# Optimization experiments

Hardware: AMD Instinct MI355X
Metric: run time of the kernel (lower is better)

## Reference

```python
import jax, jax.numpy as jnp
import numpy as np

NUM_HEADS = 8

def mha(q, k, v, in_w, in_b, out_w, out_b):
    # q:[B,Lq,E] k,v:[B,Lk,E]; torch nn.MultiheadAttention math (batch_first)
    B, Lq, E = q.shape
    Lk = k.shape[1]
    H = NUM_HEADS
    D = E // H
    wq, wk, wv = in_w[:E], in_w[E:2*E], in_w[2*E:]      # each [E,E], torch layout [out,in]
    bq, bk, bv = in_b[:E], in_b[E:2*E], in_b[2*E:]
    qp = (q @ wq.T + bq).reshape(B, Lq, H, D)
    kp = (k @ wk.T + bk).reshape(B, Lk, H, D)
    vp = (v @ wv.T + bv).reshape(B, Lk, H, D)
    scores = jnp.einsum('bqhd,bkhd->bhqk', qp, kp) / jnp.sqrt(jnp.asarray(D, q.dtype))
    attn = jax.nn.softmax(scores, axis=-1)
    ctx = jnp.einsum('bhqk,bkhd->bqhd', attn, vp).reshape(B, Lq, E)
    return ctx @ out_w.T + out_b

def setup_inputs() -> dict:
    key = jax.random.key(0)
    ks = jax.random.split(key, 12)
    B, IN, E, M, NB = 2048, 1024, 512, 256, 8
    s = lambda *d: 1.0 / np.sqrt(d[-1])
    return {
        'x':      jax.random.normal(ks[0], (B, IN), jnp.float32),
        'memory': jax.random.uniform(ks[1], (M, E), jnp.float32, -s(E), s(E)),
        'enc_w':  jax.random.uniform(ks[2], (E, IN), jnp.float32, -s(IN), s(IN)),
        'enc_b':  jnp.zeros((E,), jnp.float32),
        'blk_w':  jax.random.uniform(ks[3], (NB, E, E), jnp.float32, -s(E), s(E)),
        'blk_b':  jnp.zeros((NB, E), jnp.float32),
        'in_w':   jax.random.uniform(ks[4], (3 * E, E), jnp.float32, -s(E), s(E)),
        'in_b':   jnp.zeros((3 * E,), jnp.float32),
        'out_w':  jax.random.uniform(ks[5], (E, E), jnp.float32, -s(E), s(E)),
        'out_b':  jnp.zeros((E,), jnp.float32),
        'dec_w':  jax.random.uniform(ks[6], (IN, E), jnp.float32, -s(E), s(E)),
        'dec_b':  jnp.zeros((IN,), jnp.float32),
    }

def reference(x, memory, enc_w, enc_b, blk_w, blk_b, in_w, in_b, out_w, out_b, dec_w, dec_b):
    B = x.shape[0]
    encoded = jnp.tanh(x @ enc_w.T + enc_b)                     # [B,E]
    # all block linears at once: [B, NB, E]
    memory_updates = jnp.einsum('be,noe->bno', encoded, blk_w) + blk_b
    mem = jnp.broadcast_to(memory[None], (B,) + memory.shape)   # [B,M,E]
    attended = mha(memory_updates, mem, mem, in_w, in_b, out_w, out_b)
    updated_memory = mem + jnp.mean(attended, axis=1, keepdims=True)
    retrieved = mha(encoded[:, None, :], updated_memory, updated_memory, in_w, in_b, out_w, out_b)
    output = retrieved[:, 0, :] @ dec_w.T + dec_b               # [B,IN]
    return output, updated_memory
```

## Files before the change

### kernel.cpp

```cpp
#include <hip/hip_runtime.h>
#include <math.h>


typedef __attribute__((ext_vector_type(8))) short short8;
typedef __attribute__((ext_vector_type(4))) float f32x4;
typedef unsigned short u16;

__device__ inline u16 bf16_rn(float x) {
    unsigned u = __float_as_uint(x);
    unsigned r = (u + 0x7FFFu + ((u >> 16) & 1u)) >> 16;
    return (u16)r;
}
__device__ inline float bf16_f(u16 h) { return __uint_as_float(((unsigned)h) << 16); }

__global__ __launch_bounds__(256)
void prep_all(const float* __restrict__ x, const float* __restrict__ mm,
              const float* __restrict__ ew, const float* __restrict__ iw,
              const float* __restrict__ ow, const float* __restrict__ dw,
              const float* __restrict__ blk_w,
              const float* __restrict__ in_b, const float* __restrict__ blk_b,
              const float* __restrict__ out_b, const float* __restrict__ dec_b,
              u16* __restrict__ xh, u16* __restrict__ xl,
              u16* __restrict__ mh, u16* __restrict__ ml,
              u16* __restrict__ ewh, u16* __restrict__ ewl,
              u16* __restrict__ iwh, u16* __restrict__ iwl,
              u16* __restrict__ owh, u16* __restrict__ owl,
              u16* __restrict__ dwh, u16* __restrict__ dwl,
              u16* __restrict__ bwTh, u16* __restrict__ bwTl,
              u16* __restrict__ owTh, u16* __restrict__ owTl,
              float* __restrict__ bias1, float* __restrict__ bias2,
              float* __restrict__ bias_uv)
{
    __shared__ float T[32][33];
    const int id = blockIdx.x;
    const int t = threadIdx.x;
    if (id < 2304) {
        const int z = id >> 8, within = id & 255;
        const float* s; u16 *dh, *dl;
        if (z < 8) { s = blk_w + (long long)z * 262144;
                     dh = bwTh + (long long)z * 262144; dl = bwTl + (long long)z * 262144; }
        else       { s = ow; dh = owTh; dl = owTl; }
        const int c0 = (within & 15) * 32, r0 = (within >> 4) * 32;
        const int tx = t & 31, ty = t >> 5;
        #pragma unroll
        for (int rr = 0; rr < 4; ++rr)
            T[ty + rr * 8][tx] = s[(long long)(r0 + ty + rr * 8) * 512 + c0 + tx];
        __syncthreads();
        #pragma unroll
        for (int rr = 0; rr < 4; ++rr) {
            float v = T[tx][ty + rr * 8];
            long long o = (long long)(c0 + ty + rr * 8) * 512 + r0 + tx;
            u16 hh = bf16_rn(v);
            dh[o] = hh; dl[o] = bf16_rn(v - bf16_f(hh));
        }
    } else if (id < 2326) {
        int idx = (id - 2304) * 256 + t;
        if (idx < 4096) {
            int n = idx >> 9, f = idx & 511;
            const float* wr_ = iw + (long long)f * 512;
            const float* bb  = blk_b + n * 512;
            float s = in_b[f];
            for (int o = 0; o < 512; ++o) s += wr_[o] * bb[o];
            bias1[idx] = s;
        } else if (idx < 5120) {
            int i = idx - 4096;
            const float* dr = dw + (long long)i * 512;
            float s = dec_b[i];
            for (int f = 0; f < 512; ++f) s += dr[f] * out_b[f];
            bias2[i] = s;
        } else if (idx < 5632) {
            int f = idx - 5120;
            const float* wv = iw + (long long)(1024 + f) * 512;
            float s = 0.f;
            for (int e = 0; e < 512; ++e) s += wv[e] * out_b[e];
            bias_uv[f] = s;
        }
    } else {
        const long long total = 1081344;
        const long long stride = 2048LL * 256;
        for (long long i = (long long)(id - 2326) * 256 + t; i < total; i += stride) {
            const float* src; u16 *hi, *lo; long long j;
            if (i < 524288)      { src = x;  hi = xh;  lo = xl;  j = i; }
            else if (i < 557056) { src = mm; hi = mh;  lo = ml;  j = i - 524288; }
            else if (i < 688128) { src = ew; hi = ewh; lo = ewl; j = i - 557056; }
            else if (i < 884736) { src = iw; hi = iwh; lo = iwl; j = i - 688128; }
            else if (i < 950272) { src = ow; hi = owh; lo = owl; j = i - 884736; }
            else                 { src = dw; hi = dwh; lo = dwl; j = i - 950272; }
            float4 v = reinterpret_cast<const float4*>(src)[j];
            u16 h0 = bf16_rn(v.x), h1 = bf16_rn(v.y), h2 = bf16_rn(v.z), h3 = bf16_rn(v.w);
            ushort4 hv = {h0, h1, h2, h3};
            ushort4 lv = {bf16_rn(v.x - bf16_f(h0)), bf16_rn(v.y - bf16_f(h1)),
                          bf16_rn(v.z - bf16_f(h2)), bf16_rn(v.w - bf16_f(h3))};
            reinterpret_cast<ushort4*>(hi)[j] = hv;
            reinterpret_cast<ushort4*>(lo)[j] = lv;
        }
    }
}

struct ZD {
    const u16 *Ah, *Al, *Bh, *Bl;
    const float* bias;
    float* Cf; u16 *Ch, *Cl;
    int M, lda, ldb, ldc, K, act, omode;
    float scale;
};
template<int NZ> struct ZPack { ZD d[NZ]; };

__device__ __forceinline__ void gemm_zd(const ZD& dz, int m0, int n0,
    u16 (*Ash)[40], u16 (*Asl)[40], u16 (*Bsh)[40], u16 (*Bsl)[40])
{
    const int t  = threadIdx.x;
    const int r  = t >> 2;
    const int ck = (t & 3) << 3;
    const int lane = t & 63;
    const int wid  = t >> 6;
    const int wr = (wid >> 1) * 64;
    const int wc = (wid & 1) * 32;
    const int lr = lane & 15;
    const int lk = (lane >> 4) << 3;

    f32x4 acc[4][2];
    const f32x4 zero = {0.f, 0.f, 0.f, 0.f};
    #pragma unroll
    for (int i = 0; i < 4; ++i)
        #pragma unroll
        for (int j = 0; j < 2; ++j) acc[i][j] = zero;

    const long long arow0 = (long long)(m0 + r) * dz.lda;
    const long long arow1 = (long long)(m0 + r + 64) * dz.lda;
    const long long brow  = (long long)(n0 + r) * dz.ldb;

    for (int k0 = 0; k0 < dz.K; k0 += 32) {
        int4 vah0 = *reinterpret_cast<const int4*>(dz.Ah + arow0 + k0 + ck);
        int4 vah1 = *reinterpret_cast<const int4*>(dz.Ah + arow1 + k0 + ck);
        int4 val0 = *reinterpret_cast<const int4*>(dz.Al + arow0 + k0 + ck);
        int4 val1 = *reinterpret_cast<const int4*>(dz.Al + arow1 + k0 + ck);
        int4 vbh  = *reinterpret_cast<const int4*>(dz.Bh + brow  + k0 + ck);
        int4 vbl  = *reinterpret_cast<const int4*>(dz.Bl + brow  + k0 + ck);
        __syncthreads();
        *reinterpret_cast<int4*>(&Ash[r][ck])      = vah0;
        *reinterpret_cast<int4*>(&Ash[r + 64][ck]) = vah1;
        *reinterpret_cast<int4*>(&Asl[r][ck])      = val0;
        *reinterpret_cast<int4*>(&Asl[r + 64][ck]) = val1;
        *reinterpret_cast<int4*>(&Bsh[r][ck])      = vbh;
        *reinterpret_cast<int4*>(&Bsl[r][ck])      = vbl;
        __syncthreads();

        short8 fah[4], fal[4], fbh[2], fbl[2];
        #pragma unroll
        for (int i = 0; i < 4; ++i) {
            fah[i] = *reinterpret_cast<const short8*>(&Ash[wr + i * 16 + lr][lk]);
            fal[i] = *reinterpret_cast<const short8*>(&Asl[wr + i * 16 + lr][lk]);
        }
        #pragma unroll
        for (int j = 0; j < 2; ++j) {
            fbh[j] = *reinterpret_cast<const short8*>(&Bsh[wc + j * 16 + lr][lk]);
            fbl[j] = *reinterpret_cast<const short8*>(&Bsl[wc + j * 16 + lr][lk]);
        }
        #pragma unroll
        for (int i = 0; i < 4; ++i)
            #pragma unroll
            for (int j = 0; j < 2; ++j) {
                acc[i][j] = __builtin_amdgcn_mfma_f32_16x16x32_bf16(fah[i], fbh[j], acc[i][j], 0, 0, 0);
                acc[i][j] = __builtin_amdgcn_mfma_f32_16x16x32_bf16(fah[i], fbl[j], acc[i][j], 0, 0, 0);
                acc[i][j] = __builtin_amdgcn_mfma_f32_16x16x32_bf16(fal[i], fbh[j], acc[i][j], 0, 0, 0);
            }
    }

    #pragma unroll
    for (int j = 0; j < 2; ++j) {
        const int col = n0 + wc + j * 16 + lr;
        const float bv = dz.bias ? dz.bias[col] : 0.f;
        #pragma unroll
        for (int i = 0; i < 4; ++i) {
            #pragma unroll
            for (int q = 0; q < 4; ++q) {
                const int row = m0 + wr + i * 16 + ((lane >> 4) << 2) + q;
                float v = (acc[i][j][q] + bv) * dz.scale;
                if (dz.act) v = tanhf(v);
                if (dz.omode == 0) {
                    dz.Cf[(long long)row * dz.ldc + col] = v;
                } else {
                    long long off = (dz.omode == 1)
                        ? (long long)row * dz.ldc + col
                        : (long long)col * dz.ldc + row;
                    u16 h = bf16_rn(v);
                    dz.Ch[off] = h;
                    dz.Cl[off] = bf16_rn(v - bf16_f(h));
                }
            }
        }
    }
}

template<int NZ>
__global__ __launch_bounds__(256)
void gemm_multi(ZPack<NZ> pk)
{
    __shared__ u16 Ash[128][40];
    __shared__ u16 Asl[128][40];
    __shared__ u16 Bsh[64][40];
    __shared__ u16 Bsl[64][40];
    const ZD dz = pk.d[blockIdx.z];
    const int m0 = blockIdx.x * 128;
    if (m0 >= dz.M) return;
    gemm_zd(dz, m0, blockIdx.y * 64, Ash, Asl, Bsh, Bsl);
}

template<int MODE>
__device__ __forceinline__ void attn_body(char* smem, int bxblk, int h,
    const u16* __restrict__ Qph, const u16* __restrict__ Qpl,
    const u16* __restrict__ Kvh, const u16* __restrict__ Kvl,
    const u16* __restrict__ VTh, const u16* __restrict__ VTl,
    const float* __restrict__ uv, u16* __restrict__ Oh, u16* __restrict__ Ol)
{
    const int t = threadIdx.x;
    const int lane = t & 63, w = t >> 6;
    const int l15 = lane & 15, g = lane >> 4;
    const int wr = w * 32;
    const int b0 = bxblk * (MODE == 0 ? 16 : 128);

    u16* Qs = (u16*)smem;
    char* KsB = smem + 36864;

    for (int c = t; c < 2048; c += 256) {
        int plane = c >> 10, rem = c & 1023;
        int row = rem >> 3, seg = rem & 7;
        const u16* src = plane ? Qpl : Qph;
        long long addr;
        if (MODE == 0) {
            int q = row >> 4, bb = row & 15;
            addr = ((long long)q * 2048 + b0 + bb) * 512 + h * 64 + seg * 8;
        } else {
            addr = (long long)(b0 + row) * 512 + h * 64 + seg * 8;
        }
        *(int4*)(&Qs[plane * 9216 + row * 72 + seg * 8]) = *(const int4*)(src + addr);
    }

    f32x4 sacc[2][16];
    const f32x4 zero = {0.f, 0.f, 0.f, 0.f};
    #pragma unroll
    for (int i = 0; i < 2; ++i)
        #pragma unroll
        for (int j = 0; j < 16; ++j) sacc[i][j] = zero;

    short8 qfh[2][2], qfl[2][2];

    for (int kh = 0; kh < 2; ++kh) {
        if (kh) __syncthreads();
        for (int c = t; c < 2048; c += 256) {
            int plane = c >> 10, rem = c & 1023;
            int key = rem >> 3, seg = rem & 7;
            const u16* src = plane ? Kvl : Kvh;
            *(int4*)(KsB + plane * 18432 + key * 144 + seg * 16) =
                *(const int4*)(src + (long long)(kh * 128 + key) * 1024 + h * 64 + seg * 8);
        }
        __syncthreads();
        if (kh == 0) {
            #pragma unroll
            for (int i = 0; i < 2; ++i)
                #pragma unroll
                for (int kf = 0; kf < 2; ++kf) {
                    int ro = (wr + 16 * i + l15) * 72 + kf * 32 + g * 8;
                    qfh[i][kf] = *(const short8*)(&Qs[ro]);
                    qfl[i][kf] = *(const short8*)(&Qs[9216 + ro]);
                }
        }
        #pragma unroll
        for (int j = 0; j < 8; ++j) {
            int jg = kh * 8 + j;
            #pragma unroll
            for (int kf = 0; kf < 2; ++kf) {
                const char* kb = KsB + (j * 16 + l15) * 144 + (kf * 32 + g * 8) * 2;
                short8 kbh = *(const short8*)(kb);
                short8 kbl = *(const short8*)(kb + 18432);
                #pragma unroll
                for (int i = 0; i < 2; ++i) {
                    sacc[i][jg] = __builtin_amdgcn_mfma_f32_16x16x32_bf16(qfh[i][kf], kbh, sacc[i][jg], 0, 0, 0);
                    sacc[i][jg] = __builtin_amdgcn_mfma_f32_16x16x32_bf16(qfh[i][kf], kbl, sacc[i][jg], 0, 0, 0);
                    sacc[i][jg] = __builtin_amdgcn_mfma_f32_16x16x32_bf16(qfl[i][kf], kbh, sacc[i][jg], 0, 0, 0);
                }
            }
        }
    }

    float inv[2][4];
    #pragma unroll
    for (int i = 0; i < 2; ++i)
        #pragma unroll
        for (int q = 0; q < 4; ++q) {
            float m = -1e30f;
            #pragma unroll
            for (int j = 0; j < 16; ++j) m = fmaxf(m, sacc[i][j][q]);
            #pragma unroll
            for (int off = 1; off <= 8; off <<= 1) m = fmaxf(m, __shfl_xor(m, off, 64));
            #pragma unroll
            for (int j = 0; j < 16; ++j) sacc[i][j][q] = __expf(sacc[i][j][q] - m);
            float s = 0.f;
            #pragma unroll
            for (int j = 0; j < 16; ++j) s += sacc[i][j][q];
            #pragma unroll
            for (int off = 1; off <= 8; off <<= 1) s += __shfl_xor(s, off, 64);
            inv[i][q] = 1.0f / s;
        }

    f32x4 ctx[2][4];
    #pragma unroll
    for (int i = 0; i < 2; ++i)
        #pragma unroll
        for (int jd = 0; jd < 4; ++jd) ctx[i][jd] = zero;

    for (int qt = 0; qt < 4; ++qt) {
        __syncthreads();
        #pragma unroll
        for (int i = 0; i < 2; ++i)
            #pragma unroll
            for (int jj = 0; jj < 4; ++jj) {
                int jg = qt * 4 + jj;
                #pragma unroll
                for (int q = 0; q < 4; ++q) {
                    int row = wr + 16 * i + 4 * g + q;
                    int key = jj * 16 + l15;
                    float pv = sacc[i][jg][q];
                    u16 ph = bf16_rn(pv);
                    u16 pl = bf16_rn(pv - bf16_f(ph));
                    int byt = row * 128 + ((key * 2) ^ ((row & 7) << 4));
                    *(u16*)(smem + byt) = ph;
                    *(u16*)(smem + 16384 + byt) = pl;
                }
            }
        for (int c = t; c < 1024; c += 256) {
            int plane = c >> 9, rem = c & 511;
            int d = rem >> 3, seg = rem & 7;
            const u16* src = plane ? VTl : VTh;
            int4 v = *(const int4*)(src + (long long)h * 16384 + d * 256 + qt * 64 + seg * 8);
            int byt = 36864 + plane * 8192 + d * 128 + ((seg * 16) ^ ((d & 7) << 4));
            *(int4*)(smem + byt) = v;
        }
        __syncthreads();

        short8 pah[2][2], pal[2][2];
        #pragma unroll
        for (int i = 0; i < 2; ++i)
            #pragma unroll
            for (int kf = 0; kf < 2; ++kf) {
                int row = wr + 16 * i + l15;
                int byt = row * 128 + ((kf * 64 + g * 16) ^ ((row & 7) << 4));
                pah[i][kf] = *(const short8*)(smem + byt);
                pal[i][kf] = *(const short8*)(smem + 16384 + byt);
            }
        #pragma unroll
        for (int jd = 0; jd < 4; ++jd) {
            #pragma unroll
            for (int kf = 0; kf < 2; ++kf) {
                int d = 16 * jd + l15;
                int byt = 36864 + d * 128 + ((kf * 64 + g * 16) ^ ((d & 7) << 4));
                short8 vbh = *(const short8*)(smem + byt);
                short8 vbl = *(const short8*)(smem + 8192 + byt);
                #pragma unroll
                for (int i = 0; i < 2; ++i) {
                    ctx[i][jd] = __builtin_amdgcn_mfma_f32_16x16x32_bf16(pah[i][kf], vbh, ctx[i][jd], 0, 0, 0);
                    ctx[i][jd] = __builtin_amdgcn_mfma_f32_16x16x32_bf16(pah[i][kf], vbl, ctx[i][jd], 0, 0, 0);
                    ctx[i][jd] = __builtin_amdgcn_mfma_f32_16x16x32_bf16(pal[i][kf], vbh, ctx[i][jd], 0, 0, 0);
                }
            }
        }
    }

    if (MODE == 0) {
        __syncthreads();
        float* R = (float*)smem;
        #pragma unroll
        for (int i = 0; i < 2; ++i)
            #pragma unroll
            for (int jd = 0; jd < 4; ++jd)
                #pragma unroll
                for (int q = 0; q < 4; ++q) {
                    int qa = 2 * w + i;
                    int bb = 4 * g + q;
                    int d  = 16 * jd + l15;
                    R[qa * 1024 + bb * 64 + d] = ctx[i][jd][q] * inv[i][q];
                }
        __syncthreads();
        for (int o = t; o < 1024; o += 256) {
            int bb = o >> 6, d = o & 63;
            float s = 0.f;
            #pragma unroll
            for (int qa = 0; qa < 8; ++qa) s += R[qa * 1024 + bb * 64 + d];
            s *= 0.125f;
            long long addr = (long long)(b0 + bb) * 512 + h * 64 + d;
            u16 hh = bf16_rn(s);
            Oh[addr] = hh;
            Ol[addr] = bf16_rn(s - bf16_f(hh));
        }
    } else {
        #pragma unroll
        for (int i = 0; i < 2; ++i)
            #pragma unroll
            for (int jd = 0; jd < 4; ++jd)
                #pragma unroll
                for (int q = 0; q < 4; ++q) {
                    int b = b0 + wr + 16 * i + 4 * g + q;
                    int d = 16 * jd + l15;
                    long long addr = (long long)b * 512 + h * 64 + d;
                    float v = ctx[i][jd][q] * inv[i][q] + uv[addr];
                    u16 hh = bf16_rn(v);
                    Oh[addr] = hh;
                    Ol[addr] = bf16_rn(v - bf16_f(hh));
                }
    }
}

template<int MODE>
__global__ __launch_bounds__(256, 2)
void fused_attn(const u16* __restrict__ Qph, const u16* __restrict__ Qpl,
                const u16* __restrict__ Kvh, const u16* __restrict__ Kvl,
                const u16* __restrict__ VTh, const u16* __restrict__ VTl,
                const float* __restrict__ uv,
                u16* __restrict__ Oh, u16* __restrict__ Ol)
{
    extern __shared__ char smem[];
    attn_body<MODE>(smem, blockIdx.x, blockIdx.y, Qph, Qpl, Kvh, Kvl,
                    VTh, VTl, uv, Oh, Ol);
}

__device__ __forceinline__ void write_half(int wb, int half,
    const float* __restrict__ mem, const float* __restrict__ u,
    float* __restrict__ out1)
{
    const float4* m4 = reinterpret_cast<const float4*>(mem);
    const float4* u4 = reinterpret_cast<const float4*>(u);
    float4* o4 = reinterpret_cast<float4*>(out1);
    long long i0 = (long long)half * 33554432 + (long long)wb * 16384 + threadIdx.x;
    #pragma unroll 4
    for (int j = 0; j < 64; ++j) {
        long long i = i0 + j * 256;
        int e4 = (int)(i & 127);
        int m  = (int)((i >> 7) & 255);
        long long b = i >> 15;
        float4 a = m4[m * 128 + e4];
        float4 c = u4[b * 128 + e4];
        float4 rr = {a.x + c.x, a.y + c.y, a.z + c.z, a.w + c.w};
        o4[i] = rr;
    }
}

__global__ __launch_bounds__(256, 2)
void attn1_write(const u16* __restrict__ Qph, const u16* __restrict__ Qpl,
                 const u16* __restrict__ Kvh, const u16* __restrict__ Kvl,
                 const u16* __restrict__ VTh, const u16* __restrict__ VTl,
                 const float* __restrict__ uv,
                 u16* __restrict__ Oh, u16* __restrict__ Ol,
                 const float* __restrict__ mem, const float* __restrict__ uf,
                 float* __restrict__ out1)
{
    extern __shared__ char smem[];
    const int id = blockIdx.x;
    if (id < 128) {
        attn_body<1>(smem, id >> 3, id & 7, Qph, Qpl, Kvh, Kvl, VTh, VTl,
                     uv, Oh, Ol);
    } else {
        write_half(id - 128, 0, mem, uf, out1);
    }
}

__global__ __launch_bounds__(256)
void final_write(const u16* __restrict__ c2h, const u16* __restrict__ c2l,
                 const u16* __restrict__ W2h, const u16* __restrict__ W2l,
                 const float* __restrict__ bias2, float* __restrict__ out,
                 const float* __restrict__ mem, const float* __restrict__ uf,
                 float* __restrict__ out1)
{
    __shared__ u16 Ash[128][40];
    __shared__ u16 Asl[128][40];
    __shared__ u16 Bsh[64][40];
    __shared__ u16 Bsl[64][40];
    const int id = blockIdx.x;
    if (id < 256) {
        ZD dz = { c2h, c2l, W2h, W2l, bias2, out, nullptr, nullptr,
                  2048, 512, 512, 1024, 512, 0, 0, 1.0f };
        gemm_zd(dz, (id & 15) * 128, (id >> 4) * 64, Ash, Asl, Bsh, Bsl);
    } else {
        write_half(id - 256, 1, mem, uf, out1);
    }
}

extern "C" void kernel_launch(void* const* d_in, const int* in_sizes, int n_in,
                              void* d_out, int out_size, void* d_ws, size_t ws_size,
                              hipStream_t stream)
{
    (void)in_sizes; (void)n_in; (void)out_size; (void)ws_size;
    const float* x     = (const float*)d_in[0];
    const float* mem   = (const float*)d_in[1];
    const float* enc_w = (const float*)d_in[2];
    const float* enc_b = (const float*)d_in[3];
    const float* blk_w = (const float*)d_in[4];
    const float* blk_b = (const float*)d_in[5];
    const float* in_w  = (const float*)d_in[6];
    const float* in_b  = (const float*)d_in[7];
    const float* out_w = (const float*)d_in[8];
    const float* out_b = (const float*)d_in[9];
    const float* dec_w = (const float*)d_in[10];
    const float* dec_b = (const float*)d_in[11];
    float* out = (float*)d_out;

    char* p = (char*)d_ws;
    auto alloc = [&](size_t bytes) { char* q = p; p += (bytes + 255) & ~(size_t)255; return q; };
    u16* xh   = (u16*)alloc(2097152 * 2); u16* xl   = (u16*)alloc(2097152 * 2);
    u16* memh = (u16*)alloc(131072 * 2);  u16* meml = (u16*)alloc(131072 * 2);
    u16* ewh  = (u16*)alloc(524288 * 2);  u16* ewl  = (u16*)alloc(524288 * 2);
    u16* iwh  = (u16*)alloc(786432 * 2);  u16* iwl  = (u16*)alloc(786432 * 2);
    u16* owh  = (u16*)alloc(262144 * 2);  u16* owl  = (u16*)alloc(262144 * 2);
    u16* owTh = (u16*)alloc(262144 * 2);  u16* owTl = (u16*)alloc(262144 * 2);
    u16* dwh  = (u16*)alloc(524288 * 2);  u16* dwl  = (u16*)alloc(524288 * 2);
    u16* ench = (u16*)alloc(1048576 * 2); u16* encl = (u16*)alloc(1048576 * 2);
    u16* kvh  = (u16*)alloc(262144 * 2);  u16* kvl  = (u16*)alloc(262144 * 2);
    u16* vpTh = (u16*)alloc(131072 * 2);  u16* vpTl = (u16*)alloc(131072 * 2);
    float* bias1  = (float*)alloc(4096 * 4);
    float* bias2  = (float*)alloc(1024 * 4);
    float* biasuv = (float*)alloc(512 * 4);
    u16* cbh  = (u16*)alloc(1048576 * 2); u16* cbl  = (u16*)alloc(1048576 * 2);
    float* uf = (float*)alloc(1048576 * 4);
    u16* qp2h = (u16*)alloc(1048576 * 2); u16* qp2l = (u16*)alloc(1048576 * 2);
    float* uvb = (float*)alloc(1048576 * 4);
    u16* c2h  = (u16*)alloc(1048576 * 2); u16* c2l  = (u16*)alloc(1048576 * 2);
    u16* W2h  = (u16*)alloc(524288 * 2);  u16* W2l  = (u16*)alloc(524288 * 2);
    u16* Wuvh = (u16*)alloc(262144 * 2);  u16* Wuvl = (u16*)alloc(262144 * 2);

    float* out1 = out + 2097152;
    u16* bwTh = (u16*)out1;
    u16* bwTl = bwTh + 2097152;
    u16* W1h  = bwTl + 2097152;
    u16* W1l  = W1h + 2097152;
    u16* qp1h = W1l + 2097152;
    u16* qp1l = qp1h + 8388608;

    dim3 blk(256);

    prep_all<<<dim3(4374), blk, 0, stream>>>(x, mem, enc_w, in_w, out_w, dec_w,
        blk_w, in_b, blk_b, out_b, dec_b,
        xh, xl, memh, meml, ewh, ewl, iwh, iwl, owh, owl, dwh, dwl,
        bwTh, bwTl, owTh, owTl, bias1, bias2, biasuv);

    {
        ZPack<14> pk;
        pk.d[0] = { xh, xl, ewh, ewl, enc_b, nullptr, ench, encl,
                    2048, 1024, 1024, 512, 1024, 1, 1, 1.0f };
        for (int z = 0; z < 8; ++z)
            pk.d[1 + z] = { iwh, iwl, bwTh + (long long)z * 262144, bwTl + (long long)z * 262144,
                            nullptr, nullptr, W1h + (long long)z * 262144, W1l + (long long)z * 262144,
                            512, 512, 512, 512, 512, 0, 1, 1.0f };
        pk.d[9]  = { iwh + 1024 * 512, iwl + 1024 * 512, owTh, owTl, nullptr,
                     nullptr, Wuvh, Wuvl, 512, 512, 512, 512, 512, 0, 1, 1.0f };
        pk.d[10] = { dwh, dwl, owTh, owTl, nullptr, nullptr, W2h, W2l,
                     512, 512, 512, 512, 512, 0, 1, 1.0f };
        pk.d[11] = { dwh + 512 * 512, dwl + 512 * 512, owTh, owTl, nullptr,
                     nullptr, W2h + 512 * 512, W2l + 512 * 512,
                     512, 512, 512, 512, 512, 0, 1, 1.0f };
        pk.d[12] = { memh, meml, iwh + 512 * 512, iwl + 512 * 512, in_b + 512,
                     nullptr, kvh, kvl, 256, 512, 512, 1024, 512, 0, 1, 1.0f };
        pk.d[13] = { memh, meml, iwh + 1024 * 512, iwl + 1024 * 512, in_b + 1024,
                     nullptr, vpTh, vpTl, 256, 512, 512, 256, 512, 0, 2, 1.0f };
        gemm_multi<14><<<dim3(16, 8, 14), blk, 0, stream>>>(pk);
    }
    {
        ZPack<9> pk;
        for (int z = 0; z < 8; ++z)
            pk.d[z] = { ench, encl, W1h + (long long)z * 262144, W1l + (long long)z * 262144,
                        bias1 + z * 512, nullptr,
                        qp1h + (long long)z * 1048576, qp1l + (long long)z * 1048576,
                        2048, 512, 512, 512, 512, 0, 1, 0.125f };
        pk.d[8] = { ench, encl, iwh, iwl, in_b, nullptr, qp2h, qp2l,
                    2048, 512, 512, 512, 512, 0, 1, 0.125f };
        gemm_multi<9><<<dim3(16, 8, 9), blk, 0, stream>>>(pk);
    }
    fused_attn<0><<<dim3(128, 8), blk, 73728, stream>>>(qp1h, qp1l, kvh, kvl,
        vpTh, vpTl, nullptr, cbh, cbl);
    {
        ZPack<2> pk;
        pk.d[0] = { cbh, cbl, owh, owl, out_b, uf, nullptr, nullptr,
                    2048, 512, 512, 512, 512, 0, 0, 1.0f };
        pk.d[1] = { cbh, cbl, Wuvh, Wuvl, biasuv, uvb, nullptr, nullptr,
                    2048, 512, 512, 512, 512, 0, 0, 1.0f };
        gemm_multi<2><<<dim3(16, 8, 2), blk, 0, stream>>>(pk);
    }
    attn1_write<<<dim3(2176), blk, 73728, stream>>>(qp2h, qp2l, kvh, kvl,
        vpTh, vpTl, uvb, c2h, c2l, mem, uf, out1);
    final_write<<<dim3(2304), blk, 0, stream>>>(c2h, c2l, W2h, W2l, bias2, out,
        mem, uf, out1);
}
```

Measured before the change: 492.8 us.

## Fuse both attentions into one launch and fold uv addition into a K=1024 GEMM

The second attention no longer adds the uv term in its epilogue. It writes its context into the first half of a 1024-wide buffer, and a GEMM writes cb·Wuv into the second half. The final decoder GEMM then runs with K=1024 against a concatenated weight [dec·out_wT ; same], so it absorbs the uv addition and removes the fp32 uvb round-trip. Both attentions now run in a single launch, the broadcast write goes into one kernel with nontemporal stores, and the GEMM K-tile grows from 32 to 64, which roughly doubles LDS use per block. The final GEMM also does twice the MFMA work, in exchange for fewer launches and less memory traffic.

```diff
diff --git a/kernel.cpp b/kernel.cpp
--- a/kernel.cpp
+++ b/kernel.cpp
@@ -107,17 +107,17 @@
 template<int NZ> struct ZPack { ZD d[NZ]; };
 
 __device__ __forceinline__ void gemm_zd(const ZD& dz, int m0, int n0,
-    u16 (*Ash)[40], u16 (*Asl)[40], u16 (*Bsh)[40], u16 (*Bsl)[40])
+    u16 (*Ash)[72], u16 (*Asl)[72], u16 (*Bsh)[72], u16 (*Bsl)[72])
 {
     const int t  = threadIdx.x;
-    const int r  = t >> 2;
-    const int ck = (t & 3) << 3;
+    const int r8 = t >> 3;
+    const int ck = (t & 7) << 3;
     const int lane = t & 63;
     const int wid  = t >> 6;
     const int wr = (wid >> 1) * 64;
     const int wc = (wid & 1) * 32;
     const int lr = lane & 15;
-    const int lk = (lane >> 4) << 3;
+    const int g  = lane >> 4;
 
     f32x4 acc[4][2];
     const f32x4 zero = {0.f, 0.f, 0.f, 0.f};
@@ -126,45 +126,56 @@
         #pragma unroll
         for (int j = 0; j < 2; ++j) acc[i][j] = zero;
 
-    const long long arow0 = (long long)(m0 + r) * dz.lda;
-    const long long arow1 = (long long)(m0 + r + 64) * dz.lda;
-    const long long brow  = (long long)(n0 + r) * dz.ldb;
-
-    for (int k0 = 0; k0 < dz.K; k0 += 32) {
-        int4 vah0 = *reinterpret_cast<const int4*>(dz.Ah + arow0 + k0 + ck);
-        int4 vah1 = *reinterpret_cast<const int4*>(dz.Ah + arow1 + k0 + ck);
-        int4 val0 = *reinterpret_cast<const int4*>(dz.Al + arow0 + k0 + ck);
-        int4 val1 = *reinterpret_cast<const int4*>(dz.Al + arow1 + k0 + ck);
-        int4 vbh  = *reinterpret_cast<const int4*>(dz.Bh + brow  + k0 + ck);
-        int4 vbl  = *reinterpret_cast<const int4*>(dz.Bl + brow  + k0 + ck);
-        __syncthreads();
-        *reinterpret_cast<int4*>(&Ash[r][ck])      = vah0;
-        *reinterpret_cast<int4*>(&Ash[r + 64][ck]) = vah1;
-        *reinterpret_cast<int4*>(&Asl[r][ck])      = val0;
-        *reinterpret_cast<int4*>(&Asl[r + 64][ck]) = val1;
-        *reinterpret_cast<int4*>(&Bsh[r][ck])      = vbh;
-        *reinterpret_cast<int4*>(&Bsl[r][ck])      = vbl;
-        __syncthreads();
-
-        short8 fah[4], fal[4], fbh[2], fbl[2];
-        #pragma unroll
-        for (int i = 0; i < 4; ++i) {
-            fah[i] = *reinterpret_cast<const short8*>(&Ash[wr + i * 16 + lr][lk]);
-            fal[i] = *reinterpret_cast<const short8*>(&Asl[wr + i * 16 + lr][lk]);
-        }
-        #pragma unroll
-        for (int j = 0; j < 2; ++j) {
-            fbh[j] = *reinterpret_cast<const short8*>(&Bsh[wc + j * 16 + lr][lk]);
-            fbl[j] = *reinterpret_cast<const short8*>(&Bsl[wc + j * 16 + lr][lk]);
-        }
-        #pragma unroll
-        for (int i = 0; i < 4; ++i)
+    for (int k0 = 0; k0 < dz.K; k0 += 64) {
+        int4 vah[4], val[4], vbh[2], vbl[2];
+        #pragma unroll
+        for (int p2 = 0; p2 < 4; ++p2) {
+            long long row = (long long)(m0 + r8 + 32 * p2) * dz.lda + k0 + ck;
+            vah[p2] = *reinterpret_cast<const int4*>(dz.Ah + row);
+            val[p2] = *reinterpret_cast<const int4*>(dz.Al + row);
+        }
+        #pragma unroll
+        for (int p2 = 0; p2 < 2; ++p2) {
+            long long row = (long long)(n0 + r8 + 32 * p2) * dz.ldb + k0 + ck;
+            vbh[p2] = *reinterpret_cast<const int4*>(dz.Bh + row);
+            vbl[p2] = *reinterpret_cast<const int4*>(dz.Bl + row);
+        }
+        __syncthreads();
+        #pragma unroll
+        for (int p2 = 0; p2 < 4; ++p2) {
+            *reinterpret_cast<int4*>(&Ash[r8 + 32 * p2][ck]) = vah[p2];
+            *reinterpret_cast<int4*>(&Asl[r8 + 32 * p2][ck]) = val[p2];
+        }
+        #pragma unroll
+        for (int p2 = 0; p2 < 2; ++p2) {
+            *reinterpret_cast<int4*>(&Bsh[r8 + 32 * p2][ck]) = vbh[p2];
+            *reinterpret_cast<int4*>(&Bsl[r8 + 32 * p2][ck]) = vbl[p2];
+        }
+        __syncthreads();
+
+        #pragma unroll
+        for (int kk = 0; kk < 2; ++kk) {
+            const int lk = kk * 32 + g * 8;
+            short8 fah[4], fal[4], fbh[2], fbl[2];
+            #pragma unroll
+            for (int i = 0; i < 4; ++i) {
+                fah[i] = *reinterpret_cast<const short8*>(&Ash[wr + i * 16 + lr][lk]);
+                fal[i] = *reinterpret_cast<const short8*>(&Asl[wr + i * 16 + lr][lk]);
+            }
             #pragma unroll
             for (int j = 0; j < 2; ++j) {
-                acc[i][j] = __builtin_amdgcn_mfma_f32_16x16x32_bf16(fah[i], fbh[j], acc[i][j], 0, 0, 0);
-                acc[i][j] = __builtin_amdgcn_mfma_f32_16x16x32_bf16(fah[i], fbl[j], acc[i][j], 0, 0, 0);
-                acc[i][j] = __builtin_amdgcn_mfma_f32_16x16x32_bf16(fal[i], fbh[j], acc[i][j], 0, 0, 0);
-            }
+                fbh[j] = *reinterpret_cast<const short8*>(&Bsh[wc + j * 16 + lr][lk]);
+                fbl[j] = *reinterpret_cast<const short8*>(&Bsl[wc + j * 16 + lr][lk]);
+            }
+            #pragma unroll
+            for (int i = 0; i < 4; ++i)
+                #pragma unroll
+                for (int j = 0; j < 2; ++j) {
+                    acc[i][j] = __builtin_amdgcn_mfma_f32_16x16x32_bf16(fah[i], fbh[j], acc[i][j], 0, 0, 0);
+                    acc[i][j] = __builtin_amdgcn_mfma_f32_16x16x32_bf16(fah[i], fbl[j], acc[i][j], 0, 0, 0);
+                    acc[i][j] = __builtin_amdgcn_mfma_f32_16x16x32_bf16(fal[i], fbh[j], acc[i][j], 0, 0, 0);
+                }
+        }
     }
 
     #pragma unroll
@@ -197,10 +208,10 @@
 __global__ __launch_bounds__(256)
 void gemm_multi(ZPack<NZ> pk)
 {
-    __shared__ u16 Ash[128][40];
-    __shared__ u16 Asl[128][40];
-    __shared__ u16 Bsh[64][40];
-    __shared__ u16 Bsl[64][40];
+    __shared__ u16 Ash[128][72];
+    __shared__ u16 Asl[128][72];
+    __shared__ u16 Bsh[64][72];
+    __shared__ u16 Bsl[64][72];
     const ZD dz = pk.d[blockIdx.z];
     const int m0 = blockIdx.x * 128;
     if (m0 >= dz.M) return;
@@ -212,7 +223,7 @@
     const u16* __restrict__ Qph, const u16* __restrict__ Qpl,
     const u16* __restrict__ Kvh, const u16* __restrict__ Kvl,
     const u16* __restrict__ VTh, const u16* __restrict__ VTl,
-    const float* __restrict__ uv, u16* __restrict__ Oh, u16* __restrict__ Ol)
+    u16* __restrict__ Oh, u16* __restrict__ Ol)
 {
     const int t = threadIdx.x;
     const int lane = t & 63, w = t >> 6;
@@ -402,8 +413,8 @@
                 for (int q = 0; q < 4; ++q) {
                     int b = b0 + wr + 16 * i + 4 * g + q;
                     int d = 16 * jd + l15;
-                    long long addr = (long long)b * 512 + h * 64 + d;
-                    float v = ctx[i][jd][q] * inv[i][q] + uv[addr];
+                    long long addr = (long long)b * 1024 + h * 64 + d;
+                    float v = ctx[i][jd][q] * inv[i][q];
                     u16 hh = bf16_rn(v);
                     Oh[addr] = hh;
                     Ol[addr] = bf16_rn(v - bf16_f(hh));
@@ -411,77 +422,58 @@
     }
 }
 
-template<int MODE>
 __global__ __launch_bounds__(256, 2)
-void fused_attn(const u16* __restrict__ Qph, const u16* __restrict__ Qpl,
-                const u16* __restrict__ Kvh, const u16* __restrict__ Kvl,
-                const u16* __restrict__ VTh, const u16* __restrict__ VTl,
-                const float* __restrict__ uv,
-                u16* __restrict__ Oh, u16* __restrict__ Ol)
-{
-    extern __shared__ char smem[];
-    attn_body<MODE>(smem, blockIdx.x, blockIdx.y, Qph, Qpl, Kvh, Kvl,
-                    VTh, VTl, uv, Oh, Ol);
-}
-
-__device__ __forceinline__ void write_half(int wb, int half,
-    const float* __restrict__ mem, const float* __restrict__ u,
-    float* __restrict__ out1)
-{
-    const float4* m4 = reinterpret_cast<const float4*>(mem);
-    const float4* u4 = reinterpret_cast<const float4*>(u);
-    float4* o4 = reinterpret_cast<float4*>(out1);
-    long long i0 = (long long)half * 33554432 + (long long)wb * 16384 + threadIdx.x;
-    #pragma unroll 4
-    for (int j = 0; j < 64; ++j) {
-        long long i = i0 + j * 256;
-        int e4 = (int)(i & 127);
-        int m  = (int)((i >> 7) & 255);
-        long long b = i >> 15;
-        float4 a = m4[m * 128 + e4];
-        float4 c = u4[b * 128 + e4];
-        float4 rr = {a.x + c.x, a.y + c.y, a.z + c.z, a.w + c.w};
-        o4[i] = rr;
-    }
-}
-
-__global__ __launch_bounds__(256, 2)
-void attn1_write(const u16* __restrict__ Qph, const u16* __restrict__ Qpl,
-                 const u16* __restrict__ Kvh, const u16* __restrict__ Kvl,
-                 const u16* __restrict__ VTh, const u16* __restrict__ VTl,
-                 const float* __restrict__ uv,
-                 u16* __restrict__ Oh, u16* __restrict__ Ol,
-                 const float* __restrict__ mem, const float* __restrict__ uf,
-                 float* __restrict__ out1)
+void attn_both(const u16* __restrict__ Q1h, const u16* __restrict__ Q1l,
+               const u16* __restrict__ Q2h, const u16* __restrict__ Q2l,
+               const u16* __restrict__ Kvh, const u16* __restrict__ Kvl,
+               const u16* __restrict__ VTh, const u16* __restrict__ VTl,
+               u16* __restrict__ cbh, u16* __restrict__ cbl,
+               u16* __restrict__ ach, u16* __restrict__ acl)
 {
     extern __shared__ char smem[];
     const int id = blockIdx.x;
-    if (id < 128) {
-        attn_body<1>(smem, id >> 3, id & 7, Qph, Qpl, Kvh, Kvl, VTh, VTl,
-                     uv, Oh, Ol);
+    if (id < 1024) {
+        attn_body<0>(smem, id >> 3, id & 7, Q1h, Q1l, Kvh, Kvl, VTh, VTl,
+                     cbh, cbl);
     } else {
-        write_half(id - 128, 0, mem, uf, out1);
+        const int j = id - 1024;
+        attn_body<1>(smem, j >> 3, j & 7, Q2h, Q2l, Kvh, Kvl, VTh, VTl,
+                     ach, acl);
     }
 }
 
 __global__ __launch_bounds__(256)
-void final_write(const u16* __restrict__ c2h, const u16* __restrict__ c2l,
-                 const u16* __restrict__ W2h, const u16* __restrict__ W2l,
+void write_final(const u16* __restrict__ ach, const u16* __restrict__ acl,
+                 const u16* __restrict__ bch, const u16* __restrict__ bcl,
                  const float* __restrict__ bias2, float* __restrict__ out,
                  const float* __restrict__ mem, const float* __restrict__ uf,
                  float* __restrict__ out1)
 {
-    __shared__ u16 Ash[128][40];
-    __shared__ u16 Asl[128][40];
-    __shared__ u16 Bsh[64][40];
-    __shared__ u16 Bsl[64][40];
+    __shared__ u16 Ash[128][72];
+    __shared__ u16 Asl[128][72];
+    __shared__ u16 Bsh[64][72];
+    __shared__ u16 Bsl[64][72];
     const int id = blockIdx.x;
     if (id < 256) {
-        ZD dz = { c2h, c2l, W2h, W2l, bias2, out, nullptr, nullptr,
-                  2048, 512, 512, 1024, 512, 0, 0, 1.0f };
+        ZD dz = { ach, acl, bch, bcl, bias2, out, nullptr, nullptr,
+                  2048, 1024, 1024, 1024, 1024, 0, 0, 1.0f };
         gemm_zd(dz, (id & 15) * 128, (id >> 4) * 64, Ash, Asl, Bsh, Bsl);
     } else {
-        write_half(id - 256, 1, mem, uf, out1);
+        const f32x4* m4 = reinterpret_cast<const f32x4*>(mem);
+        const f32x4* u4 = reinterpret_cast<const f32x4*>(uf);
+        f32x4* o4 = reinterpret_cast<f32x4*>(out1);
+        long long i0 = (long long)(id - 256) * 16384 + threadIdx.x;
+        #pragma unroll 4
+        for (int j = 0; j < 64; ++j) {
+            long long i = i0 + j * 256;
+            int e4 = (int)(i & 127);
+            int m  = (int)((i >> 7) & 255);
+            long long b = i >> 15;
+            f32x4 a = m4[m * 128 + e4];
+            f32x4 c = u4[b * 128 + e4];
+            f32x4 rr = a + c;
+            __builtin_nontemporal_store(rr, &o4[i]);
+        }
     }
 }
 
@@ -522,10 +514,9 @@
     u16* cbh  = (u16*)alloc(1048576 * 2); u16* cbl  = (u16*)alloc(1048576 * 2);
     float* uf = (float*)alloc(1048576 * 4);
     u16* qp2h = (u16*)alloc(1048576 * 2); u16* qp2l = (u16*)alloc(1048576 * 2);
-    float* uvb = (float*)alloc(1048576 * 4);
-    u16* c2h  = (u16*)alloc(1048576 * 2); u16* c2l  = (u16*)alloc(1048576 * 2);
-    u16* W2h  = (u16*)alloc(524288 * 2);  u16* W2l  = (u16*)alloc(524288 * 2);
     u16* Wuvh = (u16*)alloc(262144 * 2);  u16* Wuvl = (u16*)alloc(262144 * 2);
+    u16* ach  = (u16*)alloc(2097152 * 2); u16* acl  = (u16*)alloc(2097152 * 2);
+    u16* bch  = (u16*)alloc(1048576 * 2); u16* bcl  = (u16*)alloc(1048576 * 2);
 
     float* out1 = out + 2097152;
     u16* bwTh = (u16*)out1;
@@ -543,7 +534,7 @@
         bwTh, bwTl, owTh, owTl, bias1, bias2, biasuv);
 
     {
-        ZPack<14> pk;
+        ZPack<16> pk;
         pk.d[0] = { xh, xl, ewh, ewl, enc_b, nullptr, ench, encl,
                     2048, 1024, 1024, 512, 1024, 1, 1, 1.0f };
         for (int z = 0; z < 8; ++z)
@@ -552,16 +543,18 @@
                             512, 512, 512, 512, 512, 0, 1, 1.0f };
         pk.d[9]  = { iwh + 1024 * 512, iwl + 1024 * 512, owTh, owTl, nullptr,
                      nullptr, Wuvh, Wuvl, 512, 512, 512, 512, 512, 0, 1, 1.0f };
-        pk.d[10] = { dwh, dwl, owTh, owTl, nullptr, nullptr, W2h, W2l,
-                     512, 512, 512, 512, 512, 0, 1, 1.0f };
-        pk.d[11] = { dwh + 512 * 512, dwl + 512 * 512, owTh, owTl, nullptr,
-                     nullptr, W2h + 512 * 512, W2l + 512 * 512,
-                     512, 512, 512, 512, 512, 0, 1, 1.0f };
-        pk.d[12] = { memh, meml, iwh + 512 * 512, iwl + 512 * 512, in_b + 512,
+        for (int s = 0; s < 2; ++s)
+            for (int c = 0; c < 2; ++c)
+                pk.d[10 + s * 2 + c] = { dwh + (long long)s * 262144, dwl + (long long)s * 262144,
+                                         owTh, owTl, nullptr, nullptr,
+                                         bch + (long long)s * 524288 + c * 512,
+                                         bcl + (long long)s * 524288 + c * 512,
+                                         512, 512, 512, 1024, 512, 0, 1, 1.0f };
+        pk.d[14] = { memh, meml, iwh + 512 * 512, iwl + 512 * 512, in_b + 512,
                      nullptr, kvh, kvl, 256, 512, 512, 1024, 512, 0, 1, 1.0f };
-        pk.d[13] = { memh, meml, iwh + 1024 * 512, iwl + 1024 * 512, in_b + 1024,
+        pk.d[15] = { memh, meml, iwh + 1024 * 512, iwl + 1024 * 512, in_b + 1024,
                      nullptr, vpTh, vpTl, 256, 512, 512, 256, 512, 0, 2, 1.0f };
-        gemm_multi<14><<<dim3(16, 8, 14), blk, 0, stream>>>(pk);
+        gemm_multi<16><<<dim3(16, 8, 16), blk, 0, stream>>>(pk);
     }
     {
         ZPack<9> pk;
@@ -574,18 +567,16 @@
                     2048, 512, 512, 512, 512, 0, 1, 0.125f };
         gemm_multi<9><<<dim3(16, 8, 9), blk, 0, stream>>>(pk);
     }
-    fused_attn<0><<<dim3(128, 8), blk, 73728, stream>>>(qp1h, qp1l, kvh, kvl,
-        vpTh, vpTl, nullptr, cbh, cbl);
+    attn_both<<<dim3(1152), blk, 73728, stream>>>(qp1h, qp1l, qp2h, qp2l,
+        kvh, kvl, vpTh, vpTl, cbh, cbl, ach, acl);
     {
         ZPack<2> pk;
         pk.d[0] = { cbh, cbl, owh, owl, out_b, uf, nullptr, nullptr,
                     2048, 512, 512, 512, 512, 0, 0, 1.0f };
-        pk.d[1] = { cbh, cbl, Wuvh, Wuvl, biasuv, uvb, nullptr, nullptr,
-                    2048, 512, 512, 512, 512, 0, 0, 1.0f };
+        pk.d[1] = { cbh, cbl, Wuvh, Wuvl, biasuv, nullptr, ach + 512, acl + 512,
+                    2048, 512, 512, 1024, 512, 0, 1, 1.0f };
         gemm_multi<2><<<dim3(16, 8, 2), blk, 0, stream>>>(pk);
     }
-    attn1_write<<<dim3(2176), blk, 73728, stream>>>(qp2h, qp2l, kvh, kvl,
-        vpTh, vpTl, uvb, c2h, c2l, mem, uf, out1);
-    final_write<<<dim3(2304), blk, 0, stream>>>(c2h, c2l, W2h, W2l, bias2, out,
+    write_final<<<dim3(4352), blk, 0, stream>>>(ach, acl, bch, bcl, bias2, out,
         mem, uf, out1);
 }
```

Measured after the change: 708.8 us. 43.8% more time.
